# Kernel tuning notes

Measured on AMD Instinct MI355X. Metric: run time of the kernel, lower is better.

The kernel has to match this reference:

```python
import jax, jax.numpy as jnp
import numpy as np

B, NQ, NK, DM, H, DK = 8, 1024, 1024, 512, 8, 64


def setup_inputs() -> dict:
    key = jax.random.key(0)
    ks = jax.random.split(key, 20)
    s = 1.0 / np.sqrt(DM)
    inp = {
        "queries": jax.random.normal(ks[0], (B, NQ, DM), jnp.float32),
        "keys": jax.random.normal(ks[1], (B, NK, DM), jnp.float32),
        "values": jax.random.normal(ks[2], (B, NK, DM), jnp.float32),
        "attention_mask": jax.random.randint(ks[3], (B, H, NQ, NK), 0, 2).astype(bool),
        "attention_weights": jax.random.uniform(ks[4], (B, H, NQ, NK), jnp.float32),
        "memory": jax.random.uniform(ks[5], (B, NK), jnp.float32),
        "geometry": jax.random.uniform(ks[6], (B, H, NQ, NK), jnp.float32),
        "Wq": jax.random.normal(ks[7], (DM, H * DK), jnp.float32) * s,
        "bq": jnp.zeros((H * DK,), jnp.float32),
        "Wk": jax.random.normal(ks[8], (DM, H * DK), jnp.float32) * s,
        "bk": jnp.zeros((H * DK,), jnp.float32),
        "Wv": jax.random.normal(ks[9], (DM, H * DK), jnp.float32) * s,
        "bv": jnp.zeros((H * DK,), jnp.float32),
        "Wmm": jax.random.normal(ks[10], (1, H * DK), jnp.float32),
        "bmm": jnp.zeros((H * DK,), jnp.float32),
        "Wo": jax.random.normal(ks[11], (H * DK, DM), jnp.float32) * s,
        "bo": jnp.zeros((DM,), jnp.float32),
    }
    return inp


def reference(queries, keys, values, attention_mask, attention_weights, memory,
              geometry, Wq, bq, Wk, bk, Wv, bv, Wmm, bmm, Wo, bo):
    b, nq = queries.shape[:2]
    nk = keys.shape[1]
    # projections -> (b, h, n, d)
    q = (queries @ Wq + bq).reshape(b, nq, H, DK).transpose(0, 2, 1, 3)
    k = (keys @ Wk + bk).reshape(b, nk, H, DK).transpose(0, 2, 1, 3)
    v = (values @ Wv + bv).reshape(b, nk, H, DK).transpose(0, 2, 1, 3)
    # memory gate: (b, nk, 1) @ (1, h*dk) -> (b, h, nk, dk)
    mm = (memory[..., None] @ Wmm + bmm).reshape(b, nk, H, DK).transpose(0, 2, 1, 3)
    # gated scores (b, h, nq, nk)
    att = jnp.einsum('bhqd,bhkd->bhqk', q, k * mm) / np.sqrt(DK)
    att = att * attention_weights
    att = jnp.where(attention_mask, -jnp.inf, att)
    # geometric log-bias + softmax
    w_mn = jax.nn.softmax(jnp.log(jnp.clip(geometry, 1e-6)) + att, axis=-1)
    out = jnp.einsum('bhqk,bhkd->bhqd', w_mn, v * mm)
    out = out.transpose(0, 2, 1, 3).reshape(b, nq, H * DK)
    return out @ Wo + bo
```

## Files before the change

### kernel.cpp

```cpp
#include <hip/hip_runtime.h>
#include <hip/hip_bf16.h>
#include <math.h>

#define B_ 8
#define NQ_ 1024
#define NK_ 1024
#define H_ 8
#define DK_ 64
#define HDK_ 512
#define LOG2E 1.4426950408889634f

typedef _Float16 half8 __attribute__((ext_vector_type(8)));
typedef _Float16 half4 __attribute__((ext_vector_type(4)));
typedef float f32x4 __attribute__((ext_vector_type(4)));

__global__ void detect_mask_kernel(const unsigned int* __restrict__ w, int nwords,
                                   int* __restrict__ flag) {
  __shared__ int s;
  if (threadIdx.x == 0) s = 0;
  __syncthreads();
  int bad = 0;
  for (int i = threadIdx.x; i < nwords; i += blockDim.x) {
    unsigned int v = w[i];
    if (v > 1u && v != 0x3F800000u) bad = 1;
  }
  if (bad) atomicOr(&s, 1);
  __syncthreads();
  if (threadIdx.x == 0) *flag = s;
}

__global__ __launch_bounds__(256)
void wtrans_kernel(const float* __restrict__ w0, const float* __restrict__ w1,
                   const float* __restrict__ w2, const float* __restrict__ w3,
                   _Float16* __restrict__ t0, _Float16* __restrict__ t1,
                   _Float16* __restrict__ t2, _Float16* __restrict__ t3) {
  __shared__ float tile[64][65];
  const float* W;
  _Float16* T;
  switch (blockIdx.y) {
    case 0: W = w0; T = t0; break;
    case 1: W = w1; T = t1; break;
    case 2: W = w2; T = t2; break;
    default: W = w3; T = t3; break;
  }
  const int t = blockIdx.x;
  const int k0 = (t >> 3) * 64, n0 = (t & 7) * 64;
  const int tid = threadIdx.x;
  const int r = tid >> 4, c4 = (tid & 15) * 4;
#pragma unroll
  for (int i = 0; i < 4; ++i) {
    const int kk = r + i * 16;
    float4 v = *(const float4*)(W + (size_t)(k0 + kk) * 512 + n0 + c4);
    tile[kk][c4 + 0] = v.x;
    tile[kk][c4 + 1] = v.y;
    tile[kk][c4 + 2] = v.z;
    tile[kk][c4 + 3] = v.w;
  }
  __syncthreads();
#pragma unroll
  for (int i = 0; i < 4; ++i) {
    const int nn = r + i * 16;
    half4 h;
#pragma unroll
    for (int j = 0; j < 4; ++j) h[j] = (_Float16)tile[c4 + j][nn];
    *(half4*)(T + (size_t)(n0 + nn) * 512 + k0 + c4) = h;
  }
}

__global__ __launch_bounds__(256)
void gemm_kernel(const float* __restrict__ A32, const _Float16* __restrict__ A16,
                 const _Float16* __restrict__ Bt, const float* __restrict__ bias,
                 const float* __restrict__ mem, const float* __restrict__ Wmm,
                 const float* __restrict__ bmm, void* __restrict__ outp,
                 const int mode) {
  __shared__ _Float16 As[128 * 32];
  __shared__ _Float16 Bs[128 * 32];
  const int tid = threadIdx.x;
  const int lane = tid & 63, wave = tid >> 6;
  const int wr = wave >> 1, wc = wave & 1;
  const int l15 = lane & 15, l4 = lane >> 4;
  const int row0 = blockIdx.x * 128, col0 = blockIdx.y * 128;
  const int srow = tid >> 1;
  const int sc0 = (tid & 1) * 2;

  f32x4 acc[4][4] = {};

  for (int k0 = 0; k0 < 512; k0 += 32) {
    __syncthreads();
    const _Float16* sb = Bt + (size_t)(col0 + srow) * 512 + k0;
#pragma unroll
    for (int c = 0; c < 2; ++c) {
      int ci = sc0 + c;
      half8 ha;
      if (mode == 3) {
        ha = *(const half8*)(A16 + (size_t)(row0 + srow) * 512 + k0 + ci * 8);
      } else {
        const float* s = A32 + (size_t)(row0 + srow) * 512 + k0 + ci * 8;
        float4 x = *(const float4*)s;
        float4 y = *(const float4*)(s + 4);
        ha[0] = (_Float16)x.x; ha[1] = (_Float16)x.y;
        ha[2] = (_Float16)x.z; ha[3] = (_Float16)x.w;
        ha[4] = (_Float16)y.x; ha[5] = (_Float16)y.y;
        ha[6] = (_Float16)y.z; ha[7] = (_Float16)y.w;
      }
      float4 vb = *(const float4*)(sb + ci * 8);
      int cd = ci ^ (srow & 3);
      *(half8*)((char*)As + srow * 64 + (cd << 4)) = ha;
      *(float4*)((char*)Bs + srow * 64 + (cd << 4)) = vb;
    }
    __syncthreads();
    half8 af[4], bf[4];
#pragma unroll
    for (int mi = 0; mi < 4; ++mi) {
      int r = wr * 64 + mi * 16 + l15;
      af[mi] = *(half8*)((char*)As + r * 64 + ((l4 ^ (r & 3)) << 4));
    }
#pragma unroll
    for (int ni = 0; ni < 4; ++ni) {
      int r = wc * 64 + ni * 16 + l15;
      bf[ni] = *(half8*)((char*)Bs + r * 64 + ((l4 ^ (r & 3)) << 4));
    }
#pragma unroll
    for (int mi = 0; mi < 4; ++mi)
#pragma unroll
      for (int ni = 0; ni < 4; ++ni)
        acc[mi][ni] =
            __builtin_amdgcn_mfma_f32_16x16x32_f16(af[mi], bf[ni], acc[mi][ni], 0, 0, 0);
  }

#pragma unroll
  for (int mi = 0; mi < 4; ++mi) {
#pragma unroll
    for (int ni = 0; ni < 4; ++ni) {
      const int gc = col0 + wc * 64 + ni * 16 + l15;
      const float bi = bias[gc];
      const int h = gc >> 6, d = gc & 63;
#pragma unroll
      for (int reg = 0; reg < 4; ++reg) {
        const int gr = row0 + wr * 64 + mi * 16 + l4 * 4 + reg;
        float val = acc[mi][ni][reg] + bi;
        if (mode == 3) {
          ((float*)outp)[(size_t)gr * 512 + gc] = val;
        } else if (mode == 0) {
          const int b = gr >> 10, n = gr & 1023;
          ((_Float16*)outp)[((size_t)(b * 8 + h) * 1024 + n) * 64 + d] =
              (_Float16)(val * (LOG2E / 8.0f));
        } else {
          const int b = gr >> 10, n = gr & 1023;
          float mmv = fmaf(mem[gr], Wmm[gc], bmm[gc]);
          float g = val * mmv;
          if (mode == 1)
            ((_Float16*)outp)[((size_t)(b * 8 + h) * 1024 + n) * 64 + d] = (_Float16)g;
          else
            ((_Float16*)outp)[((size_t)(b * 8 + h) * 64 + d) * 1024 + n] = (_Float16)g;
        }
      }
    }
  }
}

__global__ __launch_bounds__(256, 2)
void attn_kernel(const _Float16* __restrict__ Qp, const _Float16* __restrict__ Kg,
                 const _Float16* __restrict__ Vgt, const float* __restrict__ attw,
                 const float* __restrict__ geom, const void* __restrict__ maskp,
                 const int* __restrict__ flagp, _Float16* __restrict__ Ocat) {
  __shared__ _Float16 Kbuf[2][64 * 64];
  __shared__ _Float16 Vbuf[2][64 * 64];
  __shared__ _Float16 Ps[4][16 * 64];

  const int tid = threadIdx.x;
  const int lane = tid & 63, wave = tid >> 6;
  const int l15 = lane & 15, l4 = lane >> 4;
  const int bid = blockIdx.x;
  const int qt = bid >> 6;
  const int g = bid & 63;
  const int h = g & 7, b = g >> 3;
  const int bh = b * H_ + h;
  const int qb = qt * 64 + wave * 16;
  const int kq = qb + l15;
  const int maskBytes = *flagp;
  const unsigned char* m8 = (const unsigned char*)maskp;
  const int* m32 = (const int*)maskp;

  half8 aq[2];
  {
    const _Float16* qsrc = Qp + ((size_t)bh * NQ_ + kq) * DK_;
#pragma unroll
    for (int s = 0; s < 2; ++s) aq[s] = *(const half8*)(qsrc + s * 32 + l4 * 8);
  }

  f32x4 fo[4] = {};
  float mrun = -INFINITY, lrun = 0.f;

  const size_t wgBase = ((size_t)bh << 20) + (size_t)kq * NK_ + l4 * 4;

  const int srL = lane >> 3;
  const int sci = lane & 7;
  auto stageKV = [&](int kt, int sel) {
    const char* kgb = (const char*)(Kg + ((size_t)bh * NK_ + kt * 64) * DK_);
    const char* vgb = (const char*)(Vgt + (size_t)bh * DK_ * NK_ + kt * 64);
#pragma unroll
    for (int i = 0; i < 2; ++i) {
      const int rbase = wave * 16 + i * 8;
      const int r = rbase + srL;
      const char* src = kgb + (size_t)r * 128 + ((sci ^ (r & 7)) << 4);
      __builtin_amdgcn_global_load_lds(src, (char*)&Kbuf[sel][0] + rbase * 128, 16, 0, 0);
    }
#pragma unroll
    for (int i = 0; i < 2; ++i) {
      const int rbase = wave * 16 + i * 8;
      const int r = rbase + srL;
      const char* src = vgb + (size_t)r * (NK_ * 2) + ((sci ^ (r & 7)) << 4);
      __builtin_amdgcn_global_load_lds(src, (char*)&Vbuf[sel][0] + rbase * 128, 16, 0, 0);
    }
  };

  float4 wv[4], gv[4];
  unsigned mk;
  auto loadWG = [&](int kt) {
    const size_t base = wgBase + (size_t)kt * 64;
    unsigned m = 0;
#pragma unroll
    for (int c = 0; c < 4; ++c) {
      wv[c] = *(const float4*)(attw + base + c * 16);
      gv[c] = *(const float4*)(geom + base + c * 16);
      if (maskBytes) {
        unsigned v = *(const unsigned*)(m8 + base + c * 16);
        m |= (((v & 0xffu) ? 1u : 0u) | ((v & 0xff00u) ? 2u : 0u) |
              ((v & 0xff0000u) ? 4u : 0u) | ((v & 0xff000000u) ? 8u : 0u)) << (c * 4);
      } else {
        int4 v = *(const int4*)(m32 + base + c * 16);
        m |= ((v.x ? 1u : 0u) | (v.y ? 2u : 0u) | (v.z ? 4u : 0u) | (v.w ? 8u : 0u))
             << (c * 4);
      }
    }
    mk = m;
  };

  stageKV(0, 0);
  loadWG(0);
  __syncthreads();

#pragma unroll 2
  for (int kt = 0; kt < 16; ++kt) {
    const int sel = kt & 1;
    if (kt + 1 < 16) stageKV(kt + 1, sel ^ 1);

    const char* Kb = (const char*)&Kbuf[sel][0];
    const char* Vb = (const char*)&Vbuf[sel][0];

    f32x4 sf[4];
    __builtin_amdgcn_s_setprio(1);
#pragma unroll
    for (int c = 0; c < 4; ++c) {
      sf[c] = (f32x4){0.f, 0.f, 0.f, 0.f};
#pragma unroll
      for (int s = 0; s < 2; ++s) {
        int r = c * 16 + l15;
        half8 ak = *(half8*)(Kb + r * 128 + (((s * 4 + l4) ^ (r & 7)) << 4));
        sf[c] = __builtin_amdgcn_mfma_f32_16x16x32_f16(ak, aq[s], sf[c], 0, 0, 0);
      }
    }
    __builtin_amdgcn_s_setprio(0);

#pragma unroll
    for (int c = 0; c < 4; ++c) {
#pragma unroll
      for (int reg = 0; reg < 4; ++reg) {
        float t;
        if ((mk >> (c * 4 + reg)) & 1u)
          t = -INFINITY;
        else
          t = fmaf(sf[c][reg], wv[c][reg], __log2f(fmaxf(gv[c][reg], 1e-6f)));
        sf[c][reg] = t;
      }
    }

    if (kt + 1 < 16) loadWG(kt + 1);

    float mx = -INFINITY;
#pragma unroll
    for (int c = 0; c < 4; ++c)
#pragma unroll
      for (int reg = 0; reg < 4; ++reg) mx = fmaxf(mx, sf[c][reg]);
    mx = fmaxf(mx, __shfl_xor(mx, 16));
    mx = fmaxf(mx, __shfl_xor(mx, 32));
    float mn = fmaxf(mrun, mx);
    float sc = (mrun == -INFINITY) ? 0.f : exp2f(mrun - mn);
    mrun = mn;
    lrun *= sc;

    float scq[4];
#pragma unroll
    for (int reg = 0; reg < 4; ++reg) scq[reg] = __shfl(sc, l4 * 4 + reg);
#pragma unroll
    for (int c = 0; c < 4; ++c)
#pragma unroll
      for (int reg = 0; reg < 4; ++reg) fo[c][reg] *= scq[reg];

    float rs = 0.f;
#pragma unroll
    for (int c = 0; c < 4; ++c)
#pragma unroll
      for (int reg = 0; reg < 4; ++reg) {
        float t = sf[c][reg];
        float p = (t == -INFINITY) ? 0.f : exp2f(t - mrun);
        sf[c][reg] = p;
        rs += p;
      }
    rs += __shfl_xor(rs, 16);
    rs += __shfl_xor(rs, 32);
    lrun += rs;

    char* pw = (char*)&Ps[wave][0];
#pragma unroll
    for (int c = 0; c < 4; ++c) {
      half4 hp;
#pragma unroll
      for (int reg = 0; reg < 4; ++reg) hp[reg] = (_Float16)sf[c][reg];
      int ci = c * 2 + (l4 >> 1);
      *(half4*)(pw + l15 * 128 + ((ci ^ (l15 & 7)) << 4) + (l4 & 1) * 8) = hp;
    }

    __builtin_amdgcn_s_setprio(1);
#pragma unroll
    for (int s4 = 0; s4 < 2; ++s4) {
      half8 pa = *(half8*)(pw + l15 * 128 + (((s4 * 4 + l4) ^ (l15 & 7)) << 4));
#pragma unroll
      for (int c = 0; c < 4; ++c) {
        int rd = c * 16 + l15;
        half8 bv = *(half8*)(Vb + rd * 128 + (((s4 * 4 + l4) ^ (rd & 7)) << 4));
        fo[c] = __builtin_amdgcn_mfma_f32_16x16x32_f16(pa, bv, fo[c], 0, 0, 0);
      }
    }
    __builtin_amdgcn_s_setprio(0);

    __syncthreads();
  }

  float rinv[4];
#pragma unroll
  for (int reg = 0; reg < 4; ++reg) rinv[reg] = 1.0f / __shfl(lrun, l4 * 4 + reg);
#pragma unroll
  for (int c = 0; c < 4; ++c) {
    const int d = c * 16 + l15;
#pragma unroll
    for (int reg = 0; reg < 4; ++reg) {
      const int qg = qb + l4 * 4 + reg;
      Ocat[((size_t)b * NQ_ + qg) * HDK_ + h * DK_ + d] =
          (_Float16)(fo[c][reg] * rinv[reg]);
    }
  }
}

extern "C" void kernel_launch(void* const* d_in, const int* in_sizes, int n_in,
                              void* d_out, int out_size, void* d_ws, size_t ws_size,
                              hipStream_t stream) {
  (void)in_sizes; (void)n_in; (void)out_size; (void)ws_size;
  const float* queries = (const float*)d_in[0];
  const float* keys    = (const float*)d_in[1];
  const float* values  = (const float*)d_in[2];
  const void*  maskp   = d_in[3];
  const float* attw    = (const float*)d_in[4];
  const float* memo    = (const float*)d_in[5];
  const float* geom    = (const float*)d_in[6];
  const float* Wq = (const float*)d_in[7];
  const float* bq = (const float*)d_in[8];
  const float* Wk = (const float*)d_in[9];
  const float* bk = (const float*)d_in[10];
  const float* Wv = (const float*)d_in[11];
  const float* bv = (const float*)d_in[12];
  const float* Wmm = (const float*)d_in[13];
  const float* bmm = (const float*)d_in[14];
  const float* Wo = (const float*)d_in[15];
  const float* bo = (const float*)d_in[16];

  char* ws = (char*)d_ws;
  size_t off = 0;
  auto alloc = [&](size_t bytes) {
    char* p = ws + off;
    off += (bytes + 255) & ~(size_t)255;
    return p;
  };
  const size_t MAT = (size_t)8192 * 512 * 2;
  int* flag = (int*)alloc(256);
  _Float16* Wtq = (_Float16*)alloc((size_t)512 * 512 * 2);
  _Float16* Wtk = (_Float16*)alloc((size_t)512 * 512 * 2);
  _Float16* Wtv = (_Float16*)alloc((size_t)512 * 512 * 2);
  _Float16* Wto = (_Float16*)alloc((size_t)512 * 512 * 2);
  _Float16* Qp   = (_Float16*)alloc(MAT);
  _Float16* Kgp  = (_Float16*)alloc(MAT);
  _Float16* Vgtp = (_Float16*)alloc(MAT);
  _Float16* Ocat = (_Float16*)alloc(MAT);

  detect_mask_kernel<<<1, 256, 0, stream>>>((const unsigned int*)maskp, 4096, flag);
  wtrans_kernel<<<dim3(64, 4), 256, 0, stream>>>(Wq, Wk, Wv, Wo, Wtq, Wtk, Wtv, Wto);

  dim3 ggrid(64, 4);
  gemm_kernel<<<ggrid, 256, 0, stream>>>(queries, nullptr, Wtq, bq, nullptr, nullptr,
                                         nullptr, Qp, 0);
  gemm_kernel<<<ggrid, 256, 0, stream>>>(keys, nullptr, Wtk, bk, memo, Wmm, bmm, Kgp, 1);
  gemm_kernel<<<ggrid, 256, 0, stream>>>(values, nullptr, Wtv, bv, memo, Wmm, bmm,
                                         Vgtp, 2);

  attn_kernel<<<1024, 256, 0, stream>>>(Qp, Kgp, Vgtp, attw, geom, maskp, flag, Ocat);

  gemm_kernel<<<ggrid, 256, 0, stream>>>(nullptr, Ocat, Wto, bo, nullptr, nullptr,
                                         nullptr, d_out, 3);
}
```

Measured before the change: 339.1 us.

## Transpose PV MFMA output layout and load V fragments directly to registers

Drops the V shared-memory staging. Each wave now loads its V fragments straight from global memory into registers, and the P·V MFMA operand order is swapped so the output accumulator is laid out d-by-query. This makes the rescale factor and the row sum per-lane, which removes the shuffles for the rescale broadcast and the per-tile row-sum reduction. The final output is written as vectorized half4 stores. The cost is that the V global loads are no longer overlapped through double-buffered LDS, and each wave redundantly reads the same V tile from global/L2.

```diff
diff --git a/kernel.cpp b/kernel.cpp
--- a/kernel.cpp
+++ b/kernel.cpp
@@ -165,7 +165,6 @@
                  const float* __restrict__ geom, const void* __restrict__ maskp,
                  const int* __restrict__ flagp, _Float16* __restrict__ Ocat) {
   __shared__ _Float16 Kbuf[2][64 * 64];
-  __shared__ _Float16 Vbuf[2][64 * 64];
   __shared__ _Float16 Ps[4][16 * 64];
 
   const int tid = threadIdx.x;
@@ -193,12 +192,12 @@
   float mrun = -INFINITY, lrun = 0.f;
 
   const size_t wgBase = ((size_t)bh << 20) + (size_t)kq * NK_ + l4 * 4;
+  const _Float16* Vbase = Vgt + (size_t)bh * DK_ * NK_;
 
   const int srL = lane >> 3;
   const int sci = lane & 7;
-  auto stageKV = [&](int kt, int sel) {
+  auto stageK = [&](int kt, int sel) {
     const char* kgb = (const char*)(Kg + ((size_t)bh * NK_ + kt * 64) * DK_);
-    const char* vgb = (const char*)(Vgt + (size_t)bh * DK_ * NK_ + kt * 64);
 #pragma unroll
     for (int i = 0; i < 2; ++i) {
       const int rbase = wave * 16 + i * 8;
@@ -206,13 +205,16 @@
       const char* src = kgb + (size_t)r * 128 + ((sci ^ (r & 7)) << 4);
       __builtin_amdgcn_global_load_lds(src, (char*)&Kbuf[sel][0] + rbase * 128, 16, 0, 0);
     }
-#pragma unroll
-    for (int i = 0; i < 2; ++i) {
-      const int rbase = wave * 16 + i * 8;
-      const int r = rbase + srL;
-      const char* src = vgb + (size_t)r * (NK_ * 2) + ((sci ^ (r & 7)) << 4);
-      __builtin_amdgcn_global_load_lds(src, (char*)&Vbuf[sel][0] + rbase * 128, 16, 0, 0);
-    }
+  };
+
+  half8 vfrag[2][4];
+  auto loadV = [&](int kt) {
+#pragma unroll
+    for (int s4 = 0; s4 < 2; ++s4)
+#pragma unroll
+      for (int c = 0; c < 4; ++c)
+        vfrag[s4][c] = *(const half8*)(Vbase + (size_t)(c * 16 + l15) * NK_ +
+                                       kt * 64 + s4 * 32 + l4 * 8);
   };
 
   float4 wv[4], gv[4];
@@ -237,17 +239,17 @@
     mk = m;
   };
 
-  stageKV(0, 0);
+  stageK(0, 0);
   loadWG(0);
   __syncthreads();
 
 #pragma unroll 2
   for (int kt = 0; kt < 16; ++kt) {
     const int sel = kt & 1;
-    if (kt + 1 < 16) stageKV(kt + 1, sel ^ 1);
+    if (kt + 1 < 16) stageK(kt + 1, sel ^ 1);
+    loadV(kt);
 
     const char* Kb = (const char*)&Kbuf[sel][0];
-    const char* Vb = (const char*)&Vbuf[sel][0];
 
     f32x4 sf[4];
     __builtin_amdgcn_s_setprio(1);
@@ -285,18 +287,9 @@
       for (int reg = 0; reg < 4; ++reg) mx = fmaxf(mx, sf[c][reg]);
     mx = fmaxf(mx, __shfl_xor(mx, 16));
     mx = fmaxf(mx, __shfl_xor(mx, 32));
-    float mn = fmaxf(mrun, mx);
-    float sc = (mrun == -INFINITY) ? 0.f : exp2f(mrun - mn);
+    const float mn = fmaxf(mrun, mx);
+    const float sc = (mrun == -INFINITY) ? 0.f : exp2f(mrun - mn);
     mrun = mn;
-    lrun *= sc;
-
-    float scq[4];
-#pragma unroll
-    for (int reg = 0; reg < 4; ++reg) scq[reg] = __shfl(sc, l4 * 4 + reg);
-#pragma unroll
-    for (int c = 0; c < 4; ++c)
-#pragma unroll
-      for (int reg = 0; reg < 4; ++reg) fo[c][reg] *= scq[reg];
 
     float rs = 0.f;
 #pragma unroll
@@ -304,13 +297,15 @@
 #pragma unroll
       for (int reg = 0; reg < 4; ++reg) {
         float t = sf[c][reg];
-        float p = (t == -INFINITY) ? 0.f : exp2f(t - mrun);
+        float p = (t == -INFINITY) ? 0.f : exp2f(t - mn);
         sf[c][reg] = p;
         rs += p;
       }
-    rs += __shfl_xor(rs, 16);
-    rs += __shfl_xor(rs, 32);
-    lrun += rs;
+#pragma unroll
+    for (int c = 0; c < 4; ++c)
+#pragma unroll
+      for (int reg = 0; reg < 4; ++reg) fo[c][reg] *= sc;
+    lrun = lrun * sc + rs;
 
     char* pw = (char*)&Ps[wave][0];
 #pragma unroll
@@ -325,31 +320,28 @@
     __builtin_amdgcn_s_setprio(1);
 #pragma unroll
     for (int s4 = 0; s4 < 2; ++s4) {
-      half8 pa = *(half8*)(pw + l15 * 128 + (((s4 * 4 + l4) ^ (l15 & 7)) << 4));
-#pragma unroll
-      for (int c = 0; c < 4; ++c) {
-        int rd = c * 16 + l15;
-        half8 bv = *(half8*)(Vb + rd * 128 + (((s4 * 4 + l4) ^ (rd & 7)) << 4));
-        fo[c] = __builtin_amdgcn_mfma_f32_16x16x32_f16(pa, bv, fo[c], 0, 0, 0);
-      }
+      half8 bp = *(half8*)(pw + l15 * 128 + (((s4 * 4 + l4) ^ (l15 & 7)) << 4));
+#pragma unroll
+      for (int c = 0; c < 4; ++c)
+        fo[c] = __builtin_amdgcn_mfma_f32_16x16x32_f16(vfrag[s4][c], bp, fo[c], 0, 0, 0);
     }
     __builtin_amdgcn_s_setprio(0);
 
     __syncthreads();
   }
 
-  float rinv[4];
-#pragma unroll
-  for (int reg = 0; reg < 4; ++reg) rinv[reg] = 1.0f / __shfl(lrun, l4 * 4 + reg);
+  float lsum = lrun;
+  lsum += __shfl_xor(lsum, 16);
+  lsum += __shfl_xor(lsum, 32);
+  const float rinv = 1.0f / lsum;
+
+  _Float16* orow = Ocat + ((size_t)b * NQ_ + qb + l15) * HDK_ + h * DK_;
 #pragma unroll
   for (int c = 0; c < 4; ++c) {
-    const int d = c * 16 + l15;
-#pragma unroll
-    for (int reg = 0; reg < 4; ++reg) {
-      const int qg = qb + l4 * 4 + reg;
-      Ocat[((size_t)b * NQ_ + qg) * HDK_ + h * DK_ + d] =
-          (_Float16)(fo[c][reg] * rinv[reg]);
-    }
+    half4 hv;
+#pragma unroll
+    for (int reg = 0; reg < 4; ++reg) hv[reg] = (_Float16)(fo[c][reg] * rinv);
+    *(half4*)(orow + c * 16 + l4 * 4) = hv;
   }
 }
 
```

Result: slower. 386.9 us (+14.1%).
